# Kernel optimization log

Measured on AMD Instinct MI355X. Metric: run time of the kernel, lower is better.

## Reference

```python
import jax, jax.numpy as jnp
import numpy as np

EPS = 1e-5

def _layernorm(x, w, b):
    mu = jnp.mean(x, axis=-1, keepdims=True)
    var = jnp.mean(jnp.square(x - mu), axis=-1, keepdims=True)
    return (x - mu) * jax.lax.rsqrt(var + EPS) * w + b

def setup_inputs() -> dict:
    key = jax.random.key(0)
    ks = jax.random.split(key, 9)
    N, P_DIM, D = 16384, 3072, 1024
    patches = jax.random.normal(ks[0], (N, P_DIM), dtype=jnp.float32)
    bbox_coords = jax.random.uniform(ks[1], (N, 4), dtype=jnp.float32)
    ln1_w = jnp.ones((P_DIM,), dtype=jnp.float32)
    ln1_b = jnp.zeros((P_DIM,), dtype=jnp.float32)
    W_patch = jax.random.normal(ks[2], (D, P_DIM), dtype=jnp.float32) * (P_DIM ** -0.5)
    class_emb = jax.random.normal(ks[3], (1, 1, D), dtype=jnp.float32)
    W_pos = jax.random.normal(ks[4], (D, 4), dtype=jnp.float32) * 0.5
    b_pos = jax.random.normal(ks[5], (D,), dtype=jnp.float32) * 0.02
    class_pos = jax.random.normal(ks[6], (1, D), dtype=jnp.float32)
    return {"patches": patches, "bbox_coords": bbox_coords, "ln1_w": ln1_w,
            "ln1_b": ln1_b, "W_patch": W_patch, "class_emb": class_emb,
            "W_pos": W_pos, "b_pos": b_pos, "class_pos": class_pos}

def reference(patches, bbox_coords, ln1_w, ln1_b, W_patch, class_emb, W_pos, b_pos, class_pos):
    # Batched equivalent of the per-patch loop: LayerNorm -> Linear (no bias).
    # NOTE: torch code computes patch_norm2 but appends the PRE-norm2 embedding,
    # so norm2 is dead code and omitted here.
    x = _layernorm(patches, ln1_w, ln1_b)                      # [N, patch_dim]
    patch_embeds = jnp.einsum('np,dp->nd', x, W_patch)          # [N, D]
    embeddings = jnp.concatenate([class_emb, patch_embeds[None]], axis=1)  # [1, N+1, D]
    pos = jnp.einsum('nc,dc->nd', bbox_coords, W_pos) + b_pos   # [N, D]
    pos_full = jnp.concatenate([class_pos[None], pos[None]], axis=1)       # [1, N+1, D]
    return embeddings + pos_full
```

## Files before the change

kernel.cpp:

```cpp
#include <hip/hip_runtime.h>

typedef unsigned short u16;
typedef __attribute__((ext_vector_type(8))) short bf16x8;
typedef __attribute__((ext_vector_type(16))) float f32x16;

#define AS1C(p) ((const __attribute__((address_space(1))) void*)(p))
#define AS3(p)  ((__attribute__((address_space(3))) void*)(p))

__device__ __forceinline__ u16 f2bf(float f) {
    unsigned u = __float_as_uint(f);
    u += 0x7fffu + ((u >> 16) & 1u);
    return (u16)(u >> 16);
}

__global__ __launch_bounds__(256) void prep_kernel(
    const float* __restrict__ x, const float* __restrict__ w,
    const float* __restrict__ b, const float* __restrict__ Wp,
    const float* __restrict__ ce, const float* __restrict__ cp,
    u16* __restrict__ A, u16* __restrict__ Wb, float* __restrict__ out,
    int N, int D, int K)
{
    const int blk = blockIdx.x;
    const int t = threadIdx.x;

    if (blk < N) {
        const float* xr = x + (size_t)blk * K;
        float4 v[3];
#pragma unroll
        for (int i = 0; i < 3; ++i)
            v[i] = *(const float4*)&xr[(i * 256 + t) * 4];

        float s = 0.f;
#pragma unroll
        for (int i = 0; i < 3; ++i) s += v[i].x + v[i].y + v[i].z + v[i].w;
#pragma unroll
        for (int off = 32; off; off >>= 1) s += __shfl_down(s, off);

        __shared__ float red[8];
        const int wid = t >> 6, lane = t & 63;
        if (lane == 0) red[wid] = s;
        __syncthreads();
        const float mu = (red[0] + red[1] + red[2] + red[3]) * (1.0f / 3072.0f);

        float sq = 0.f;
#pragma unroll
        for (int i = 0; i < 3; ++i) {
            float dx = v[i].x - mu, dy = v[i].y - mu, dz = v[i].z - mu, dw = v[i].w - mu;
            sq += dx * dx + dy * dy + dz * dz + dw * dw;
        }
#pragma unroll
        for (int off = 32; off; off >>= 1) sq += __shfl_down(sq, off);
        if (lane == 0) red[4 + wid] = sq;
        __syncthreads();
        const float var = (red[4] + red[5] + red[6] + red[7]) * (1.0f / 3072.0f);
        const float inv = rsqrtf(var + 1e-5f);

#pragma unroll
        for (int i = 0; i < 3; ++i) {
            const int j = (i * 256 + t) * 4;
            const float4 wv = *(const float4*)&w[j];
            const float4 bv = *(const float4*)&b[j];
            ushort4 o;
            o.x = f2bf((v[i].x - mu) * inv * wv.x + bv.x);
            o.y = f2bf((v[i].y - mu) * inv * wv.y + bv.y);
            o.z = f2bf((v[i].z - mu) * inv * wv.z + bv.z);
            o.w = f2bf((v[i].w - mu) * inv * wv.w + bv.w);
            *(ushort4*)&A[(size_t)blk * K + j] = o;
        }
    } else if (blk < N + D) {
        const int row = blk - N;
        const float* wr = Wp + (size_t)row * K;
#pragma unroll
        for (int i = 0; i < 3; ++i) {
            const int j = (i * 256 + t) * 4;
            const float4 v = *(const float4*)&wr[j];
            ushort4 o;
            o.x = f2bf(v.x); o.y = f2bf(v.y); o.z = f2bf(v.z); o.w = f2bf(v.w);
            *(ushort4*)&Wb[(size_t)row * K + j] = o;
        }
    } else {
#pragma unroll
        for (int i = 0; i < 4; ++i) {
            const int j = i * 256 + t;
            out[j] = ce[j] + cp[j];
        }
    }
}

#define STG_A(BUFOFS, R0, T_) \
    __builtin_amdgcn_global_load_lds(AS1C(aS + (size_t)(R0) * 3072 + (T_) * 64), \
                                     AS3(dA + (BUFOFS) + (R0) * 128), 16, 0, 0)
#define STG_B(BUFOFS, R0, T_) \
    __builtin_amdgcn_global_load_lds(AS1C(bS + (size_t)(R0) * 3072 + (T_) * 64), \
                                     AS3(dB + (BUFOFS) + (R0) * 128), 16, 0, 0)

#define MFMA32(d, a, b) d = __builtin_amdgcn_mfma_f32_32x32x16_bf16(a, b, d, 0, 0, 0)

#define PHASE5(BUF, CK, STG, WT) do {                                             \
    const char* Lb = L + (BUF);                                                   \
    bf16x8 a0 = *(const bf16x8*)(Lb + aRowBase + 0 * 4096 + (CK));                \
    bf16x8 a1 = *(const bf16x8*)(Lb + aRowBase + 1 * 4096 + (CK));                \
    bf16x8 a2 = *(const bf16x8*)(Lb + aRowBase + 2 * 4096 + (CK));                \
    bf16x8 a3 = *(const bf16x8*)(Lb + aRowBase + 3 * 4096 + (CK));                \
    bf16x8 b0 = *(const bf16x8*)(Lb + bRowBase + 0 * 4096 + (CK));                \
    bf16x8 b1 = *(const bf16x8*)(Lb + bRowBase + 1 * 4096 + (CK));                \
    STG;                                                                          \
    __builtin_amdgcn_s_barrier();                                                 \
    asm volatile("s_waitcnt lgkmcnt(0)" ::: "memory");                            \
    __builtin_amdgcn_s_setprio(1);                                                \
    MFMA32(acc[0][0], a0, b0); MFMA32(acc[1][0], a1, b0);                         \
    MFMA32(acc[2][0], a2, b0); MFMA32(acc[3][0], a3, b0);                         \
    MFMA32(acc[0][1], a0, b1); MFMA32(acc[1][1], a1, b1);                         \
    MFMA32(acc[2][1], a2, b1); MFMA32(acc[3][1], a3, b1);                         \
    __builtin_amdgcn_s_setprio(0);                                                \
    WT;                                                                           \
    __builtin_amdgcn_s_barrier();                                                 \
} while (0)

__global__ __launch_bounds__(512, 2) void gemm_256_8ph_kernel(
    const u16* __restrict__ A, const u16* __restrict__ W,
    const float* __restrict__ bbox, const float* __restrict__ Wpos,
    const float* __restrict__ bpos, float* __restrict__ out,
    int D)
{
    __shared__ __align__(16) char lds[131072];
    const char* L = (const char*)lds;
    const int K = 3072;
    const int NK = 48;

    const int bid = blockIdx.x;
    const int swb = (bid & 7) * 32 + (bid >> 3);
    const int bx = swb & 3;
    const int by = swb >> 2;
    const int brow = by * 256;
    const int bcol = bx * 256;

    const int t = threadIdx.x;
    const int wid = t >> 6, lane = t & 63;
    const int wm = wid >> 2;
    const int wn = wid & 3;
    const int l31 = lane & 31;
    const int klane16 = (lane >> 5) * 16;
    const int xorb = (lane & 7) << 4;
    const int aRowBase = (wm * 128 + l31) * 128;
    const int bRowBase = 32768 + (wn * 64 + l31) * 128;
    const int ck0 = (0  + klane16) ^ xorb;
    const int ck1 = (32 + klane16) ^ xorb;
    const int ck2 = (64 + klane16) ^ xorb;
    const int ck3 = (96 + klane16) ^ xorb;

    const int srow = t >> 3;
    const int scol = ((t & 7) ^ ((t >> 3) & 7)) * 8;
    const u16* aS = A + (size_t)(brow + srow) * K + scol;
    const u16* bS = W + (size_t)(bcol + srow) * K + scol;
    char* dA = (char*)lds + t * 16;
    char* dB = (char*)lds + 32768 + t * 16;

    f32x16 acc[4][2] = {};

    STG_A(0, 0, 0);   STG_A(0, 64, 0);  STG_A(0, 128, 0); STG_A(0, 192, 0);
    STG_B(0, 0, 0);   STG_B(0, 64, 0);  STG_B(0, 128, 0); STG_B(0, 192, 0);
    STG_A(65536, 0, 1); STG_A(65536, 128, 1);
    asm volatile("s_waitcnt vmcnt(2)" ::: "memory");
    __builtin_amdgcn_s_barrier();

    for (int T = 0; T < NK; T += 2) {
        const bool more = (T + 2) < NK;
        PHASE5(0, ck0, { STG_A(65536, 64, T + 1); STG_A(65536, 192, T + 1); }, ((void)0));
        PHASE5(0, ck1, { STG_B(65536, 0, T + 1); STG_B(65536, 64, T + 1); }, ((void)0));
        PHASE5(0, ck2, { STG_B(65536, 128, T + 1); STG_B(65536, 192, T + 1); }, ((void)0));
        PHASE5(0, ck3,
              { if (more) { STG_A(0, 0, T + 2); STG_A(0, 128, T + 2); } },
              { if (more) asm volatile("s_waitcnt vmcnt(2)" ::: "memory");
                else      asm volatile("s_waitcnt vmcnt(0)" ::: "memory"); });
        PHASE5(65536, ck0, { if (more) { STG_A(0, 64, T + 2); STG_A(0, 192, T + 2); } }, ((void)0));
        PHASE5(65536, ck1, { if (more) { STG_B(0, 0, T + 2); STG_B(0, 64, T + 2); } }, ((void)0));
        PHASE5(65536, ck2, { if (more) { STG_B(0, 128, T + 2); STG_B(0, 192, T + 2); } }, ((void)0));
        PHASE5(65536, ck3,
              { if (more) { STG_A(65536, 0, T + 3); STG_A(65536, 128, T + 3); } },
              { asm volatile("s_waitcnt vmcnt(2)" ::: "memory"); });
    }

    float* Lf = (float*)lds;
    const int lrofs = (lane >> 5) * 4;
    const int cg = bcol + lane * 4;

    float4 wpv[4];
    float bpv[4];
#pragma unroll
    for (int j = 0; j < 4; ++j) {
        wpv[j] = *(const float4*)&Wpos[(cg + j) * 4];
        bpv[j] = bpos[cg + j];
    }

#pragma unroll
    for (int mb = 0; mb < 4; ++mb) {
        __builtin_amdgcn_s_barrier();
#pragma unroll
        for (int nb = 0; nb < 2; ++nb) {
            const int cc = wn * 64 + nb * 32 + l31;
#pragma unroll
            for (int reg = 0; reg < 16; ++reg) {
                const int frow = (reg & 3) + 8 * (reg >> 2) + lrofs;
                Lf[(wm * 32 + frow) * 256 + cc] = acc[mb][nb][reg];
            }
        }
        __builtin_amdgcn_s_barrier();
#pragma unroll
        for (int i = 0; i < 8; ++i) {
            const int lrow = wid + 8 * i;
            const int gr = brow + (lrow >> 5) * 128 + mb * 32 + (lrow & 31);
            const float4 v = *(const float4*)&Lf[lrow * 256 + lane * 4];
            const float4 bb = *(const float4*)&bbox[(size_t)gr * 4];
            float4 o;
            o.x = v.x + bpv[0] + bb.x * wpv[0].x + bb.y * wpv[0].y + bb.z * wpv[0].z + bb.w * wpv[0].w;
            o.y = v.y + bpv[1] + bb.x * wpv[1].x + bb.y * wpv[1].y + bb.z * wpv[1].z + bb.w * wpv[1].w;
            o.z = v.z + bpv[2] + bb.x * wpv[2].x + bb.y * wpv[2].y + bb.z * wpv[2].z + bb.w * wpv[2].w;
            o.w = v.w + bpv[3] + bb.x * wpv[3].x + bb.y * wpv[3].y + bb.z * wpv[3].z + bb.w * wpv[3].w;
            *(float4*)&out[(size_t)(gr + 1) * D + cg] = o;
        }
    }
}

extern "C" void kernel_launch(void* const* d_in, const int* in_sizes, int n_in,
                              void* d_out, int out_size, void* d_ws, size_t ws_size,
                              hipStream_t stream)
{
    const float* patches   = (const float*)d_in[0];
    const float* bbox      = (const float*)d_in[1];
    const float* ln1_w     = (const float*)d_in[2];
    const float* ln1_b     = (const float*)d_in[3];
    const float* W_patch   = (const float*)d_in[4];
    const float* class_emb = (const float*)d_in[5];
    const float* W_pos     = (const float*)d_in[6];
    const float* b_pos     = (const float*)d_in[7];
    const float* class_pos = (const float*)d_in[8];
    float* out = (float*)d_out;

    const int N = in_sizes[1] / 4;
    const int K = in_sizes[2];
    const int D = in_sizes[7];

    u16* Abf = (u16*)d_ws;
    u16* Wbf = Abf + (size_t)N * K;

    prep_kernel<<<N + D + 1, 256, 0, stream>>>(patches, ln1_w, ln1_b, W_patch,
                                               class_emb, class_pos, Abf, Wbf, out,
                                               N, D, K);

    const int nblk = (N / 256) * (D / 256);
    gemm_256_8ph_kernel<<<nblk, 512, 0, stream>>>(Abf, Wbf, bbox, W_pos, b_pos, out, D);
}
```

Before: 160.6 us.

## Restructure GEMM main loop into M-half phases with fewer barriers per tile

Replaces the eight per-K-chunk phases per double-tile with four phases, each covering one M-half across all four K-chunks. Each phase loads A/B fragments for two K-chunks, runs MFMAs, then loads the next two while issuing four global-to-LDS stages per phase. This halves the number of block barriers and changes fragment reuse: B fragments are reloaded for each M-half. LDS read traffic rises and the second half's LDS loads are exposed, with no barrier overlap for them.

```diff
diff --git a/kernel.cpp b/kernel.cpp
--- a/kernel.cpp
+++ b/kernel.cpp
@@ -96,28 +96,46 @@
 
 #define MFMA32(d, a, b) d = __builtin_amdgcn_mfma_f32_32x32x16_bf16(a, b, d, 0, 0, 0)
 
-#define PHASE5(BUF, CK, STG, WT) do {                                             \
-    const char* Lb = L + (BUF);                                                   \
-    bf16x8 a0 = *(const bf16x8*)(Lb + aRowBase + 0 * 4096 + (CK));                \
-    bf16x8 a1 = *(const bf16x8*)(Lb + aRowBase + 1 * 4096 + (CK));                \
-    bf16x8 a2 = *(const bf16x8*)(Lb + aRowBase + 2 * 4096 + (CK));                \
-    bf16x8 a3 = *(const bf16x8*)(Lb + aRowBase + 3 * 4096 + (CK));                \
-    bf16x8 b0 = *(const bf16x8*)(Lb + bRowBase + 0 * 4096 + (CK));                \
-    bf16x8 b1 = *(const bf16x8*)(Lb + bRowBase + 1 * 4096 + (CK));                \
+#define PHMH(BUF, MH, STG, WT) do {                                               \
+    const char* Ab = L + (BUF) + aRowBase + (MH) * 8192;                          \
+    const char* Bb = L + (BUF) + bRowBase;                                        \
+    bf16x8 x0 = *(const bf16x8*)(Ab + 0    + ck0);                                \
+    bf16x8 x1 = *(const bf16x8*)(Ab + 4096 + ck0);                                \
+    bf16x8 y0 = *(const bf16x8*)(Bb + 0    + ck0);                                \
+    bf16x8 y1 = *(const bf16x8*)(Bb + 4096 + ck0);                                \
+    bf16x8 x2 = *(const bf16x8*)(Ab + 0    + ck1);                                \
+    bf16x8 x3 = *(const bf16x8*)(Ab + 4096 + ck1);                                \
+    bf16x8 y2 = *(const bf16x8*)(Bb + 0    + ck1);                                \
+    bf16x8 y3 = *(const bf16x8*)(Bb + 4096 + ck1);                                \
     STG;                                                                          \
     __builtin_amdgcn_s_barrier();                                                 \
     asm volatile("s_waitcnt lgkmcnt(0)" ::: "memory");                            \
     __builtin_amdgcn_s_setprio(1);                                                \
-    MFMA32(acc[0][0], a0, b0); MFMA32(acc[1][0], a1, b0);                         \
-    MFMA32(acc[2][0], a2, b0); MFMA32(acc[3][0], a3, b0);                         \
-    MFMA32(acc[0][1], a0, b1); MFMA32(acc[1][1], a1, b1);                         \
-    MFMA32(acc[2][1], a2, b1); MFMA32(acc[3][1], a3, b1);                         \
+    MFMA32(acc[(MH)*2+0][0], x0, y0); MFMA32(acc[(MH)*2+1][0], x1, y0);           \
+    MFMA32(acc[(MH)*2+0][1], x0, y1); MFMA32(acc[(MH)*2+1][1], x1, y1);           \
+    MFMA32(acc[(MH)*2+0][0], x2, y2); MFMA32(acc[(MH)*2+1][0], x3, y2);           \
+    MFMA32(acc[(MH)*2+0][1], x2, y3); MFMA32(acc[(MH)*2+1][1], x3, y3);           \
+    __builtin_amdgcn_s_setprio(0);                                                \
+    bf16x8 z0 = *(const bf16x8*)(Ab + 0    + ck2);                                \
+    bf16x8 z1 = *(const bf16x8*)(Ab + 4096 + ck2);                                \
+    bf16x8 w0 = *(const bf16x8*)(Bb + 0    + ck2);                                \
+    bf16x8 w1 = *(const bf16x8*)(Bb + 4096 + ck2);                                \
+    bf16x8 z2 = *(const bf16x8*)(Ab + 0    + ck3);                                \
+    bf16x8 z3 = *(const bf16x8*)(Ab + 4096 + ck3);                                \
+    bf16x8 w2 = *(const bf16x8*)(Bb + 0    + ck3);                                \
+    bf16x8 w3 = *(const bf16x8*)(Bb + 4096 + ck3);                                \
+    asm volatile("s_waitcnt lgkmcnt(0)" ::: "memory");                            \
+    __builtin_amdgcn_s_setprio(1);                                                \
+    MFMA32(acc[(MH)*2+0][0], z0, w0); MFMA32(acc[(MH)*2+1][0], z1, w0);           \
+    MFMA32(acc[(MH)*2+0][1], z0, w1); MFMA32(acc[(MH)*2+1][1], z1, w1);           \
+    MFMA32(acc[(MH)*2+0][0], z2, w2); MFMA32(acc[(MH)*2+1][0], z3, w2);           \
+    MFMA32(acc[(MH)*2+0][1], z2, w3); MFMA32(acc[(MH)*2+1][1], z3, w3);           \
     __builtin_amdgcn_s_setprio(0);                                                \
     WT;                                                                           \
     __builtin_amdgcn_s_barrier();                                                 \
 } while (0)
 
-__global__ __launch_bounds__(512, 2) void gemm_256_8ph_kernel(
+__global__ __launch_bounds__(512, 2) void gemm_256_mh_kernel(
     const u16* __restrict__ A, const u16* __restrict__ W,
     const float* __restrict__ bbox, const float* __restrict__ Wpos,
     const float* __restrict__ bpos, float* __restrict__ out,
@@ -166,19 +184,23 @@
 
     for (int T = 0; T < NK; T += 2) {
         const bool more = (T + 2) < NK;
-        PHASE5(0, ck0, { STG_A(65536, 64, T + 1); STG_A(65536, 192, T + 1); }, ((void)0));
-        PHASE5(0, ck1, { STG_B(65536, 0, T + 1); STG_B(65536, 64, T + 1); }, ((void)0));
-        PHASE5(0, ck2, { STG_B(65536, 128, T + 1); STG_B(65536, 192, T + 1); }, ((void)0));
-        PHASE5(0, ck3,
-              { if (more) { STG_A(0, 0, T + 2); STG_A(0, 128, T + 2); } },
-              { if (more) asm volatile("s_waitcnt vmcnt(2)" ::: "memory");
-                else      asm volatile("s_waitcnt vmcnt(0)" ::: "memory"); });
-        PHASE5(65536, ck0, { if (more) { STG_A(0, 64, T + 2); STG_A(0, 192, T + 2); } }, ((void)0));
-        PHASE5(65536, ck1, { if (more) { STG_B(0, 0, T + 2); STG_B(0, 64, T + 2); } }, ((void)0));
-        PHASE5(65536, ck2, { if (more) { STG_B(0, 128, T + 2); STG_B(0, 192, T + 2); } }, ((void)0));
-        PHASE5(65536, ck3,
-              { if (more) { STG_A(65536, 0, T + 3); STG_A(65536, 128, T + 3); } },
-              { asm volatile("s_waitcnt vmcnt(2)" ::: "memory"); });
+        PHMH(0, 0,
+             { STG_B(65536, 0, T + 1); STG_B(65536, 64, T + 1);
+               STG_A(65536, 64, T + 1); STG_A(65536, 192, T + 1); },
+             ((void)0));
+        PHMH(0, 1,
+             { STG_B(65536, 128, T + 1); STG_B(65536, 192, T + 1);
+               if (more) { STG_A(0, 0, T + 2); STG_A(0, 128, T + 2); } },
+             { if (more) asm volatile("s_waitcnt vmcnt(2)" ::: "memory");
+               else      asm volatile("s_waitcnt vmcnt(0)" ::: "memory"); });
+        PHMH(65536, 0,
+             { if (more) { STG_A(0, 64, T + 2); STG_A(0, 192, T + 2);
+                           STG_B(0, 0, T + 2); STG_B(0, 64, T + 2); } },
+             ((void)0));
+        PHMH(65536, 1,
+             { if (more) { STG_B(0, 128, T + 2); STG_B(0, 192, T + 2);
+                           STG_A(65536, 0, T + 3); STG_A(65536, 128, T + 3); } },
+             { if (more) asm volatile("s_waitcnt vmcnt(2)" ::: "memory"); });
     }
 
     float* Lf = (float*)lds;
@@ -249,5 +271,5 @@
                                                N, D, K);
 
     const int nblk = (N / 256) * (D / 256);
-    gemm_256_8ph_kernel<<<nblk, 512, 0, stream>>>(Abf, Wbf, bbox, W_pos, b_pos, out, D);
-}
+    gemm_256_mh_kernel<<<nblk, 512, 0, stream>>>(Abf, Wbf, bbox, W_pos, b_pos, out, D);
+}
```

New measurement: 160.4 us. Within noise of the previous version (-0.1%).

## Switch GEMM to 16x16x32 MFMA with reordered K-half load pipeline

Applied to the files above, without the earlier changes.

Replaces the 32x32x16 bf16 MFMA tiling with 16x16x32 MFMAs. Each wave now holds 8x4 accumulator fragments, and each phase computes half of the M rows over half of the 128-wide K tile. The global-to-LDS staging schedule is reordered: B is loaded before A, the prologue waits for all loads, and the vmcnt waits are changed. The intent is a more favorable MFMA shape and fewer LDS reads per FLOP. The cost is more MFMA instructions and a shallower prefetch overlap in the prologue.

```diff
diff --git a/kernel.cpp b/kernel.cpp
--- a/kernel.cpp
+++ b/kernel.cpp
@@ -2,10 +2,12 @@
 
 typedef unsigned short u16;
 typedef __attribute__((ext_vector_type(8))) short bf16x8;
-typedef __attribute__((ext_vector_type(16))) float f32x16;
+typedef __attribute__((ext_vector_type(4))) float f32x4;
 
 #define AS1C(p) ((const __attribute__((address_space(1))) void*)(p))
 #define AS3(p)  ((__attribute__((address_space(3))) void*)(p))
+
+#define CFENCE() asm volatile("" ::: "memory")
 
 __device__ __forceinline__ u16 f2bf(float f) {
     unsigned u = __float_as_uint(f);
@@ -94,30 +96,39 @@
     __builtin_amdgcn_global_load_lds(AS1C(bS + (size_t)(R0) * 3072 + (T_) * 64), \
                                      AS3(dB + (BUFOFS) + (R0) * 128), 16, 0, 0)
 
-#define MFMA32(d, a, b) d = __builtin_amdgcn_mfma_f32_32x32x16_bf16(a, b, d, 0, 0, 0)
-
-#define PHASE5(BUF, CK, STG, WT) do {                                             \
-    const char* Lb = L + (BUF);                                                   \
-    bf16x8 a0 = *(const bf16x8*)(Lb + aRowBase + 0 * 4096 + (CK));                \
-    bf16x8 a1 = *(const bf16x8*)(Lb + aRowBase + 1 * 4096 + (CK));                \
-    bf16x8 a2 = *(const bf16x8*)(Lb + aRowBase + 2 * 4096 + (CK));                \
-    bf16x8 a3 = *(const bf16x8*)(Lb + aRowBase + 3 * 4096 + (CK));                \
-    bf16x8 b0 = *(const bf16x8*)(Lb + bRowBase + 0 * 4096 + (CK));                \
-    bf16x8 b1 = *(const bf16x8*)(Lb + bRowBase + 1 * 4096 + (CK));                \
+#define MFMA16(d, a, b) d = __builtin_amdgcn_mfma_f32_16x16x32_bf16(a, b, d, 0, 0, 0)
+
+#define PH16(BUF, MH, KH, STG, WT) do {                                           \
+    const char* Ab = L + (BUF) + aRowBase + (MH) * 8192;                          \
+    const char* Bb = L + (BUF) + bRowBase;                                        \
+    const int ck = (KH) ? ckh1 : ckh0;                                            \
+    bf16x8 a0 = *(const bf16x8*)(Ab + 0 * 2048 + ck);                             \
+    bf16x8 a1 = *(const bf16x8*)(Ab + 1 * 2048 + ck);                             \
+    bf16x8 a2 = *(const bf16x8*)(Ab + 2 * 2048 + ck);                             \
+    bf16x8 a3 = *(const bf16x8*)(Ab + 3 * 2048 + ck);                             \
+    bf16x8 b0 = *(const bf16x8*)(Bb + 0 * 2048 + ck);                             \
+    bf16x8 b1 = *(const bf16x8*)(Bb + 1 * 2048 + ck);                             \
+    bf16x8 b2 = *(const bf16x8*)(Bb + 2 * 2048 + ck);                             \
+    bf16x8 b3 = *(const bf16x8*)(Bb + 3 * 2048 + ck);                             \
     STG;                                                                          \
     __builtin_amdgcn_s_barrier();                                                 \
     asm volatile("s_waitcnt lgkmcnt(0)" ::: "memory");                            \
     __builtin_amdgcn_s_setprio(1);                                                \
-    MFMA32(acc[0][0], a0, b0); MFMA32(acc[1][0], a1, b0);                         \
-    MFMA32(acc[2][0], a2, b0); MFMA32(acc[3][0], a3, b0);                         \
-    MFMA32(acc[0][1], a0, b1); MFMA32(acc[1][1], a1, b1);                         \
-    MFMA32(acc[2][1], a2, b1); MFMA32(acc[3][1], a3, b1);                         \
+    MFMA16(acc[(MH)*4+0][0], a0, b0); MFMA16(acc[(MH)*4+0][1], a0, b1);           \
+    MFMA16(acc[(MH)*4+0][2], a0, b2); MFMA16(acc[(MH)*4+0][3], a0, b3);           \
+    MFMA16(acc[(MH)*4+1][0], a1, b0); MFMA16(acc[(MH)*4+1][1], a1, b1);           \
+    MFMA16(acc[(MH)*4+1][2], a1, b2); MFMA16(acc[(MH)*4+1][3], a1, b3);           \
+    MFMA16(acc[(MH)*4+2][0], a2, b0); MFMA16(acc[(MH)*4+2][1], a2, b1);           \
+    MFMA16(acc[(MH)*4+2][2], a2, b2); MFMA16(acc[(MH)*4+2][3], a2, b3);           \
+    MFMA16(acc[(MH)*4+3][0], a3, b0); MFMA16(acc[(MH)*4+3][1], a3, b1);           \
+    MFMA16(acc[(MH)*4+3][2], a3, b2); MFMA16(acc[(MH)*4+3][3], a3, b3);           \
     __builtin_amdgcn_s_setprio(0);                                                \
     WT;                                                                           \
     __builtin_amdgcn_s_barrier();                                                 \
+    CFENCE();                                                                     \
 } while (0)
 
-__global__ __launch_bounds__(512, 2) void gemm_256_8ph_kernel(
+__global__ __launch_bounds__(512, 2) void gemm_256_cnt_kernel(
     const u16* __restrict__ A, const u16* __restrict__ W,
     const float* __restrict__ bbox, const float* __restrict__ Wpos,
     const float* __restrict__ bpos, float* __restrict__ out,
@@ -139,15 +150,13 @@
     const int wid = t >> 6, lane = t & 63;
     const int wm = wid >> 2;
     const int wn = wid & 3;
-    const int l31 = lane & 31;
-    const int klane16 = (lane >> 5) * 16;
-    const int xorb = (lane & 7) << 4;
-    const int aRowBase = (wm * 128 + l31) * 128;
-    const int bRowBase = 32768 + (wn * 64 + l31) * 128;
-    const int ck0 = (0  + klane16) ^ xorb;
-    const int ck1 = (32 + klane16) ^ xorb;
-    const int ck2 = (64 + klane16) ^ xorb;
-    const int ck3 = (96 + klane16) ^ xorb;
+    const int fr = lane & 15;
+    const int kq16 = ((lane >> 4) & 3) * 16;
+    const int xorb = (fr & 7) << 4;
+    const int aRowBase = (wm * 128 + fr) * 128;
+    const int bRowBase = 32768 + (wn * 64 + fr) * 128;
+    const int ckh0 = (0  + kq16) ^ xorb;
+    const int ckh1 = (64 + kq16) ^ xorb;
 
     const int srow = t >> 3;
     const int scol = ((t & 7) ^ ((t >> 3) & 7)) * 8;
@@ -156,33 +165,33 @@
     char* dA = (char*)lds + t * 16;
     char* dB = (char*)lds + 32768 + t * 16;
 
-    f32x16 acc[4][2] = {};
-
-    STG_A(0, 0, 0);   STG_A(0, 64, 0);  STG_A(0, 128, 0); STG_A(0, 192, 0);
+    f32x4 acc[8][4] = {};
+
     STG_B(0, 0, 0);   STG_B(0, 64, 0);  STG_B(0, 128, 0); STG_B(0, 192, 0);
-    STG_A(65536, 0, 1); STG_A(65536, 128, 1);
-    asm volatile("s_waitcnt vmcnt(2)" ::: "memory");
+    STG_A(0, 0, 0);   STG_A(0, 128, 0); STG_A(0, 64, 0);  STG_A(0, 192, 0);
+    asm volatile("s_waitcnt vmcnt(0)" ::: "memory");
     __builtin_amdgcn_s_barrier();
+    CFENCE();
 
     for (int T = 0; T < NK; T += 2) {
         const bool more = (T + 2) < NK;
-        PHASE5(0, ck0, { STG_A(65536, 64, T + 1); STG_A(65536, 192, T + 1); }, ((void)0));
-        PHASE5(0, ck1, { STG_B(65536, 0, T + 1); STG_B(65536, 64, T + 1); }, ((void)0));
-        PHASE5(0, ck2, { STG_B(65536, 128, T + 1); STG_B(65536, 192, T + 1); }, ((void)0));
-        PHASE5(0, ck3,
-              { if (more) { STG_A(0, 0, T + 2); STG_A(0, 128, T + 2); } },
-              { if (more) asm volatile("s_waitcnt vmcnt(2)" ::: "memory");
-                else      asm volatile("s_waitcnt vmcnt(0)" ::: "memory"); });
-        PHASE5(65536, ck0, { if (more) { STG_A(0, 64, T + 2); STG_A(0, 192, T + 2); } }, ((void)0));
-        PHASE5(65536, ck1, { if (more) { STG_B(0, 0, T + 2); STG_B(0, 64, T + 2); } }, ((void)0));
-        PHASE5(65536, ck2, { if (more) { STG_B(0, 128, T + 2); STG_B(0, 192, T + 2); } }, ((void)0));
-        PHASE5(65536, ck3,
-              { if (more) { STG_A(65536, 0, T + 3); STG_A(65536, 128, T + 3); } },
-              { asm volatile("s_waitcnt vmcnt(2)" ::: "memory"); });
+        PH16(0, 0, 0, { STG_B(65536, 0, T + 1); STG_B(65536, 64, T + 1); }, ((void)0));
+        PH16(0, 0, 1, { STG_B(65536, 128, T + 1); STG_B(65536, 192, T + 1); },
+             { asm volatile("s_waitcnt vmcnt(4)" ::: "memory"); });
+        PH16(0, 1, 0, { STG_A(65536, 0, T + 1); STG_A(65536, 128, T + 1); }, ((void)0));
+        PH16(0, 1, 1, { STG_A(65536, 64, T + 1); STG_A(65536, 192, T + 1); },
+             { asm volatile("s_waitcnt vmcnt(2)" ::: "memory"); });
+        PH16(65536, 0, 0, { if (more) { STG_B(0, 0, T + 2); STG_B(0, 64, T + 2); } }, ((void)0));
+        PH16(65536, 0, 1, { if (more) { STG_B(0, 128, T + 2); STG_B(0, 192, T + 2); } },
+             { if (more) asm volatile("s_waitcnt vmcnt(4)" ::: "memory");
+               else      asm volatile("s_waitcnt vmcnt(0)" ::: "memory"); });
+        PH16(65536, 1, 0, { if (more) { STG_A(0, 0, T + 2); STG_A(0, 128, T + 2); } }, ((void)0));
+        PH16(65536, 1, 1, { if (more) { STG_A(0, 64, T + 2); STG_A(0, 192, T + 2); } },
+             { if (more) asm volatile("s_waitcnt vmcnt(2)" ::: "memory"); });
     }
 
     float* Lf = (float*)lds;
-    const int lrofs = (lane >> 5) * 4;
+    const int r4 = ((lane >> 4) & 3) * 4;
     const int cg = bcol + lane * 4;
 
     float4 wpv[4];
@@ -194,22 +203,26 @@
     }
 
 #pragma unroll
-    for (int mb = 0; mb < 4; ++mb) {
+    for (int c = 0; c < 4; ++c) {
         __builtin_amdgcn_s_barrier();
-#pragma unroll
-        for (int nb = 0; nb < 2; ++nb) {
-            const int cc = wn * 64 + nb * 32 + l31;
-#pragma unroll
-            for (int reg = 0; reg < 16; ++reg) {
-                const int frow = (reg & 3) + 8 * (reg >> 2) + lrofs;
-                Lf[(wm * 32 + frow) * 256 + cc] = acc[mb][nb][reg];
+        CFENCE();
+#pragma unroll
+        for (int q = 0; q < 2; ++q) {
+#pragma unroll
+            for (int n = 0; n < 4; ++n) {
+                const f32x4 v = acc[c * 2 + q][n];
+                const int col = wn * 64 + n * 16 + fr;
+#pragma unroll
+                for (int r = 0; r < 4; ++r)
+                    Lf[(wm * 32 + q * 16 + r4 + r) * 256 + col] = v[r];
             }
         }
         __builtin_amdgcn_s_barrier();
+        CFENCE();
 #pragma unroll
         for (int i = 0; i < 8; ++i) {
             const int lrow = wid + 8 * i;
-            const int gr = brow + (lrow >> 5) * 128 + mb * 32 + (lrow & 31);
+            const int gr = brow + (lrow >> 5) * 128 + c * 32 + (lrow & 31);
             const float4 v = *(const float4*)&Lf[lrow * 256 + lane * 4];
             const float4 bb = *(const float4*)&bbox[(size_t)gr * 4];
             float4 o;
@@ -249,5 +262,5 @@
                                                N, D, K);
 
     const int nblk = (N / 256) * (D / 256);
-    gemm_256_8ph_kernel<<<nblk, 512, 0, stream>>>(Abf, Wbf, bbox, W_pos, b_pos, out, D);
-}
+    gemm_256_cnt_kernel<<<nblk, 512, 0, stream>>>(Abf, Wbf, bbox, W_pos, b_pos, out, D);
+}
```

Result: faster. 156.1 us (-2.8%).

## Split LDS waits in GEMM phases and rebalance global-to-LDS prefetch schedule

Applied to the files above, without the earlier changes.

Each MFMA phase now drops the mid-phase barrier and waits on LDS reads in two steps (lgkmcnt 2 then 0), so the first half of the MFMAs starts while the a2/a3 fragments are still loading. The global-to-LDS staging is redistributed over three phases per buffer with a full vmcnt(0) drain at the end of each half-iteration, replacing the earlier vmcnt(2) scheme with A rows prefetched two tiles ahead. Compiler fences and sched_barriers are added to stop the scheduler from reordering across the waits. This aims to hide LDS latency behind MFMA work, at the cost of a shallower global prefetch that could expose memory latency.

```diff
diff --git a/kernel.cpp b/kernel.cpp
--- a/kernel.cpp
+++ b/kernel.cpp
@@ -6,6 +6,8 @@
 
 #define AS1C(p) ((const __attribute__((address_space(1))) void*)(p))
 #define AS3(p)  ((__attribute__((address_space(3))) void*)(p))
+
+#define CFENCE() asm volatile("" ::: "memory")
 
 __device__ __forceinline__ u16 f2bf(float f) {
     unsigned u = __float_as_uint(f);
@@ -96,28 +98,33 @@
 
 #define MFMA32(d, a, b) d = __builtin_amdgcn_mfma_f32_32x32x16_bf16(a, b, d, 0, 0, 0)
 
-#define PHASE5(BUF, CK, STG, WT) do {                                             \
-    const char* Lb = L + (BUF);                                                   \
-    bf16x8 a0 = *(const bf16x8*)(Lb + aRowBase + 0 * 4096 + (CK));                \
-    bf16x8 a1 = *(const bf16x8*)(Lb + aRowBase + 1 * 4096 + (CK));                \
-    bf16x8 a2 = *(const bf16x8*)(Lb + aRowBase + 2 * 4096 + (CK));                \
-    bf16x8 a3 = *(const bf16x8*)(Lb + aRowBase + 3 * 4096 + (CK));                \
-    bf16x8 b0 = *(const bf16x8*)(Lb + bRowBase + 0 * 4096 + (CK));                \
-    bf16x8 b1 = *(const bf16x8*)(Lb + bRowBase + 1 * 4096 + (CK));                \
+#define LGKM(N_) asm volatile("s_waitcnt lgkmcnt(" #N_ ")" ::: "memory"); \
+                 __builtin_amdgcn_sched_barrier(0)
+
+#define PH32(BUF, CK, STG, WT) do {                                               \
+    const char* Ab = L + (BUF) + aRowBase;                                        \
+    const char* Bb = L + (BUF) + bRowBase;                                        \
+    bf16x8 a0 = *(const bf16x8*)(Ab + 0 * 4096 + (CK));                           \
+    bf16x8 a1 = *(const bf16x8*)(Ab + 1 * 4096 + (CK));                           \
+    bf16x8 b0 = *(const bf16x8*)(Bb + 0 * 4096 + (CK));                           \
+    bf16x8 b1 = *(const bf16x8*)(Bb + 1 * 4096 + (CK));                           \
+    bf16x8 a2 = *(const bf16x8*)(Ab + 2 * 4096 + (CK));                           \
+    bf16x8 a3 = *(const bf16x8*)(Ab + 3 * 4096 + (CK));                           \
     STG;                                                                          \
-    __builtin_amdgcn_s_barrier();                                                 \
-    asm volatile("s_waitcnt lgkmcnt(0)" ::: "memory");                            \
     __builtin_amdgcn_s_setprio(1);                                                \
+    LGKM(2);                                                                      \
     MFMA32(acc[0][0], a0, b0); MFMA32(acc[1][0], a1, b0);                         \
+    MFMA32(acc[0][1], a0, b1); MFMA32(acc[1][1], a1, b1);                         \
+    LGKM(0);                                                                      \
     MFMA32(acc[2][0], a2, b0); MFMA32(acc[3][0], a3, b0);                         \
-    MFMA32(acc[0][1], a0, b1); MFMA32(acc[1][1], a1, b1);                         \
     MFMA32(acc[2][1], a2, b1); MFMA32(acc[3][1], a3, b1);                         \
     __builtin_amdgcn_s_setprio(0);                                                \
     WT;                                                                           \
     __builtin_amdgcn_s_barrier();                                                 \
+    CFENCE();                                                                     \
 } while (0)
 
-__global__ __launch_bounds__(512, 2) void gemm_256_8ph_kernel(
+__global__ __launch_bounds__(512, 2) void gemm_256_r13_kernel(
     const u16* __restrict__ A, const u16* __restrict__ W,
     const float* __restrict__ bbox, const float* __restrict__ Wpos,
     const float* __restrict__ bpos, float* __restrict__ out,
@@ -158,27 +165,28 @@
 
     f32x16 acc[4][2] = {};
 
-    STG_A(0, 0, 0);   STG_A(0, 64, 0);  STG_A(0, 128, 0); STG_A(0, 192, 0);
     STG_B(0, 0, 0);   STG_B(0, 64, 0);  STG_B(0, 128, 0); STG_B(0, 192, 0);
-    STG_A(65536, 0, 1); STG_A(65536, 128, 1);
-    asm volatile("s_waitcnt vmcnt(2)" ::: "memory");
+    STG_A(0, 0, 0);   STG_A(0, 128, 0); STG_A(0, 64, 0);  STG_A(0, 192, 0);
+    asm volatile("s_waitcnt vmcnt(0)" ::: "memory");
     __builtin_amdgcn_s_barrier();
+    CFENCE();
 
     for (int T = 0; T < NK; T += 2) {
         const bool more = (T + 2) < NK;
-        PHASE5(0, ck0, { STG_A(65536, 64, T + 1); STG_A(65536, 192, T + 1); }, ((void)0));
-        PHASE5(0, ck1, { STG_B(65536, 0, T + 1); STG_B(65536, 64, T + 1); }, ((void)0));
-        PHASE5(0, ck2, { STG_B(65536, 128, T + 1); STG_B(65536, 192, T + 1); }, ((void)0));
-        PHASE5(0, ck3,
-              { if (more) { STG_A(0, 0, T + 2); STG_A(0, 128, T + 2); } },
-              { if (more) asm volatile("s_waitcnt vmcnt(2)" ::: "memory");
-                else      asm volatile("s_waitcnt vmcnt(0)" ::: "memory"); });
-        PHASE5(65536, ck0, { if (more) { STG_A(0, 64, T + 2); STG_A(0, 192, T + 2); } }, ((void)0));
-        PHASE5(65536, ck1, { if (more) { STG_B(0, 0, T + 2); STG_B(0, 64, T + 2); } }, ((void)0));
-        PHASE5(65536, ck2, { if (more) { STG_B(0, 128, T + 2); STG_B(0, 192, T + 2); } }, ((void)0));
-        PHASE5(65536, ck3,
-              { if (more) { STG_A(65536, 0, T + 3); STG_A(65536, 128, T + 3); } },
-              { asm volatile("s_waitcnt vmcnt(2)" ::: "memory"); });
+        PH32(0, ck0, { STG_B(65536, 0, T + 1); STG_B(65536, 64, T + 1);
+                       STG_B(65536, 128, T + 1); }, ((void)0));
+        PH32(0, ck1, { STG_B(65536, 192, T + 1); STG_A(65536, 0, T + 1);
+                       STG_A(65536, 128, T + 1); }, ((void)0));
+        PH32(0, ck2, { STG_A(65536, 64, T + 1); STG_A(65536, 192, T + 1); }, ((void)0));
+        PH32(0, ck3, ((void)0),
+             { asm volatile("s_waitcnt vmcnt(0)" ::: "memory"); });
+        PH32(65536, ck0, { if (more) { STG_B(0, 0, T + 2); STG_B(0, 64, T + 2);
+                                       STG_B(0, 128, T + 2); } }, ((void)0));
+        PH32(65536, ck1, { if (more) { STG_B(0, 192, T + 2); STG_A(0, 0, T + 2);
+                                       STG_A(0, 128, T + 2); } }, ((void)0));
+        PH32(65536, ck2, { if (more) { STG_A(0, 64, T + 2); STG_A(0, 192, T + 2); } }, ((void)0));
+        PH32(65536, ck3, ((void)0),
+             { if (more) asm volatile("s_waitcnt vmcnt(0)" ::: "memory"); });
     }
 
     float* Lf = (float*)lds;
@@ -196,6 +204,7 @@
 #pragma unroll
     for (int mb = 0; mb < 4; ++mb) {
         __builtin_amdgcn_s_barrier();
+        CFENCE();
 #pragma unroll
         for (int nb = 0; nb < 2; ++nb) {
             const int cc = wn * 64 + nb * 32 + l31;
@@ -206,6 +215,7 @@
             }
         }
         __builtin_amdgcn_s_barrier();
+        CFENCE();
 #pragma unroll
         for (int i = 0; i < 8; ++i) {
             const int lrow = wid + 8 * i;
@@ -249,5 +259,5 @@
                                                N, D, K);
 
     const int nblk = (N / 256) * (D / 256);
-    gemm_256_8ph_kernel<<<nblk, 512, 0, stream>>>(Abf, Wbf, bbox, W_pos, b_pos, out, D);
-}
+    gemm_256_r13_kernel<<<nblk, 512, 0, stream>>>(Abf, Wbf, bbox, W_pos, b_pos, out, D);
+}
```

Measured after the change: 157.8 us. Within noise of the previous version (-1.7%).
